# Optimization experiments

Measured on AMD Instinct MI355X. Metric: run time of the kernel, lower is better.

The kernel has to match this reference:

```python
import jax, jax.numpy as jnp
import numpy as np

N_NODES = 100000
N_EDGES = 1600000
DIM_IN, DIM_H, DIM_OUT = 128, 128, 64


def setup_inputs() -> dict:
    key = jax.random.key(0)
    ks = jax.random.split(key, 8)
    s = 0.05
    return {
        "x": jax.random.normal(ks[0], (N_NODES, DIM_IN), jnp.float32),
        "edge_index": jax.random.randint(ks[1], (2, N_EDGES), 0, N_NODES, jnp.int64),
        "W_l1": jax.random.normal(ks[2], (DIM_IN, DIM_H), jnp.float32) * s,
        "W_r1": jax.random.normal(ks[3], (DIM_IN, DIM_H), jnp.float32) * s,
        "b1": jax.random.normal(ks[4], (DIM_H,), jnp.float32) * s,
        "W_l2": jax.random.normal(ks[5], (DIM_H, DIM_OUT), jnp.float32) * s,
        "W_r2": jax.random.normal(ks[6], (DIM_H, DIM_OUT), jnp.float32) * s,
        "b2": jax.random.normal(ks[7], (DIM_OUT,), jnp.float32) * s,
    }


def _sage_conv(h, src, dst, n_nodes, W_l, W_r, b):
    # mean-aggregate neighbor features: gather x[src], scatter-sum to dst, divide by in-degree
    msg = h[src]                                              # [E, d]
    agg = jax.ops.segment_sum(msg, dst, num_segments=n_nodes)  # [N, d]
    deg = jax.ops.segment_sum(jnp.ones((src.shape[0],), h.dtype), dst, num_segments=n_nodes)
    mean = agg / jnp.maximum(deg, 1.0)[:, None]
    # out = lin_l(mean) + lin_r(x) ; bias lives on lin_l (PyG SAGEConv default)
    return mean @ W_l + h @ W_r + b


def reference(x, edge_index, W_l1, W_r1, b1, W_l2, W_r2, b2):
    src, dst = edge_index[0], edge_index[1]
    n = x.shape[0]
    h = jax.nn.relu(_sage_conv(x, src, dst, n, W_l1, W_r1, b1))
    # dropout(p=0.5) is identity in eval mode
    return _sage_conv(h, src, dst, n, W_l2, W_r2, b2)
```

## Files before the change

kernel.cpp:

```cpp
#include <hip/hip_runtime.h>

#define NN 100000
#define NE 1600000

typedef __attribute__((ext_vector_type(8))) short bf16x8;
typedef __attribute__((ext_vector_type(4))) float f32x4;

__device__ __forceinline__ float bf2f(unsigned short b) {
    union { unsigned int u; float f; } v;
    v.u = ((unsigned int)b) << 16;
    return v.f;
}
__device__ __forceinline__ unsigned short f2bf(float f) {
    union { float f; unsigned int u; } v; v.f = f;
    unsigned int u = v.u;
    return (unsigned short)((u + 0x7FFFu + ((u >> 16) & 1u)) >> 16);
}

__global__ void detect_kernel(const int* __restrict__ e, int* __restrict__ flag) {
    int t = blockIdx.x * blockDim.x + threadIdx.x;
    if (t < 4096 && e[2 * t + 1] != 0) atomicOr(flag, 1);
}

__device__ __forceinline__ int esrc(const int* e, int mode, int i) {
    return mode ? e[i] : e[2 * i];
}
__device__ __forceinline__ int edst(const int* e, int mode, int i) {
    return mode ? e[NE + i] : e[2 * (NE + i)];
}

#define NRANGE 4
#define RSZ 25000
#define NCHUNK 64
#define EPC (NE / NCHUNK)
#define GS 100352
#define RECCAP 8192

__global__ __launch_bounds__(512) void histA_kernel(
    const int* __restrict__ e, const int* __restrict__ flag,
    int* __restrict__ G, int2* __restrict__ recs, int* __restrict__ cnt) {
    __shared__ int lh[RSZ];
    __shared__ int lcnt;
    const int bid = blockIdx.x;
    const int r = bid & (NRANGE - 1);
    const int c = bid >> 2;
    const int lo = r * RSZ;
    for (int idx = threadIdx.x; idx < RSZ; idx += 512) lh[idx] = 0;
    if (threadIdx.x == 0) lcnt = 0;
    __syncthreads();
    const int mode = *flag;
    const int base = c * EPC;
    int2* __restrict__ myrec = recs + (size_t)bid * RECCAP;
    for (int i = base + threadIdx.x; i < base + EPC; i += 512) {
        int dl = edst(e, mode, i) - lo;
        if ((unsigned)dl < (unsigned)RSZ) {
            int s = esrc(e, mode, i);
            int p = atomicAdd(&lh[dl], 1);
            int slot = atomicAdd(&lcnt, 1);
            if (slot < RECCAP) myrec[slot] = make_int2(dl | (p << 15), s);
        }
    }
    __syncthreads();
    for (int idx = threadIdx.x; idx < RSZ; idx += 512)
        G[(size_t)c * GS + lo + idx] = lh[idx];
    if (threadIdx.x == 0) cnt[bid] = lcnt;
}

#define PREF_B 391
#define CVT_G 6250

__global__ __launch_bounds__(256) void prefix_cvt_kernel(
    int* __restrict__ G, int* __restrict__ S,
    const float* __restrict__ xin, unsigned short* __restrict__ xb) {
    if (blockIdx.x < PREF_B) {
        int d = blockIdx.x * 256 + threadIdx.x;
        if (d >= NN) return;
        int run = 0;
#pragma unroll 8
        for (int c = 0; c < NCHUNK; c++) {
            size_t idx = (size_t)c * GS + d;
            int t = G[idx];
            G[idx] = run;
            run += t;
        }
        S[d] = run;
    } else {
        long long i = ((long long)(blockIdx.x - PREF_B) * 256 + threadIdx.x) * 8;
        float4 a = *(const float4*)(xin + i);
        float4 b = *(const float4*)(xin + i + 4);
        bf16x8 rv;
        rv[0] = (short)f2bf(a.x); rv[1] = (short)f2bf(a.y);
        rv[2] = (short)f2bf(a.z); rv[3] = (short)f2bf(a.w);
        rv[4] = (short)f2bf(b.x); rv[5] = (short)f2bf(b.y);
        rv[6] = (short)f2bf(b.z); rv[7] = (short)f2bf(b.w);
        *(bf16x8*)(xb + i) = rv;
    }
}

#define SCAN_G 392

__global__ __launch_bounds__(256) void blocksum_kernel(const int* __restrict__ S,
                                                       int* __restrict__ part) {
    int i = blockIdx.x * 256 + threadIdx.x;
    int v = (i < NN) ? S[i] : 0;
#pragma unroll
    for (int off = 32; off; off >>= 1) v += __shfl_down(v, off, 64);
    __shared__ int wsum[4];
    if ((threadIdx.x & 63) == 0) wsum[threadIdx.x >> 6] = v;
    __syncthreads();
    if (threadIdx.x == 0)
        part[blockIdx.x] = wsum[0] + wsum[1] + wsum[2] + wsum[3];
}

__global__ __launch_bounds__(512) void partscan_kernel(int* __restrict__ part) {
    __shared__ int lds[512];
    const int t = threadIdx.x;
    int v = (t < SCAN_G) ? part[t] : 0;
    lds[t] = v;
    __syncthreads();
    for (int off = 1; off < 512; off <<= 1) {
        int u = (t >= off) ? lds[t - off] : 0;
        __syncthreads();
        lds[t] += u;
        __syncthreads();
    }
    if (t < SCAN_G) part[t] = lds[t] - v;
}

__global__ __launch_bounds__(256) void scanfin_kernel(int* __restrict__ S,
                                                      const int* __restrict__ part) {
    __shared__ int lds[256];
    const int t = threadIdx.x;
    const int i = blockIdx.x * 256 + t;
    int v = (i < NN) ? S[i] : 0;
    lds[t] = v;
    __syncthreads();
    for (int off = 1; off < 256; off <<= 1) {
        int u = (t >= off) ? lds[t - off] : 0;
        __syncthreads();
        lds[t] += u;
        __syncthreads();
    }
    if (i < NN) S[i] = lds[t] - v + part[blockIdx.x];
}

__global__ __launch_bounds__(512) void fillC_kernel(
    const int* __restrict__ S, const int* __restrict__ G,
    const int2* __restrict__ recs, const int* __restrict__ cnt,
    int* __restrict__ csr) {
    __shared__ int sOff[RSZ];
    const int bid = blockIdx.x;
    const int r = bid & (NRANGE - 1);
    const int c = bid >> 2;
    const int lo = r * RSZ;
    for (int idx = threadIdx.x; idx < RSZ; idx += 512)
        sOff[idx] = S[lo + idx] + G[(size_t)c * GS + lo + idx];
    __syncthreads();
    const int n = cnt[bid];
    const int2* __restrict__ myrec = recs + (size_t)bid * RECCAP;
    for (int k = threadIdx.x; k < n; k += 512) {
        int2 rec = myrec[k];
        int dl = rec.x & 0x7FFF;
        int p = rec.x >> 15;
        csr[sOff[dl] + p] = rec.y;
    }
}

template <int D>
__global__ __launch_bounds__(256) void gather_mean_bf16(
    const unsigned short* __restrict__ feat, const int* __restrict__ csr,
    const int* __restrict__ S, unsigned short* __restrict__ out) {
    constexpr int TPN = D / 8;
    constexpr int NPB = 256 / TPN;
    const int tid = threadIdx.x;
    const int node = blockIdx.x * NPB + tid / TPN;
    const int c = tid % TPN;
    if (node >= NN) return;
    const int begin = S[node];
    const int end = (node == NN - 1) ? NE : S[node + 1];
    float acc0[8] = {0.f, 0.f, 0.f, 0.f, 0.f, 0.f, 0.f, 0.f};
    float acc1[8] = {0.f, 0.f, 0.f, 0.f, 0.f, 0.f, 0.f, 0.f};
    int j = begin;
    for (; j + 4 <= end; j += 4) {
        int s0 = csr[j], s1 = csr[j + 1], s2 = csr[j + 2], s3 = csr[j + 3];
        bf16x8 v0 = *(const bf16x8*)(feat + (size_t)s0 * D + 8 * c);
        bf16x8 v1 = *(const bf16x8*)(feat + (size_t)s1 * D + 8 * c);
        bf16x8 v2 = *(const bf16x8*)(feat + (size_t)s2 * D + 8 * c);
        bf16x8 v3 = *(const bf16x8*)(feat + (size_t)s3 * D + 8 * c);
#pragma unroll
        for (int q = 0; q < 8; q++) {
            acc0[q] += bf2f((unsigned short)v0[q]) + bf2f((unsigned short)v2[q]);
            acc1[q] += bf2f((unsigned short)v1[q]) + bf2f((unsigned short)v3[q]);
        }
    }
    for (; j < end; j++) {
        int s = csr[j];
        bf16x8 v = *(const bf16x8*)(feat + (size_t)s * D + 8 * c);
#pragma unroll
        for (int q = 0; q < 8; q++) acc0[q] += bf2f((unsigned short)v[q]);
    }
    const float inv = 1.0f / fmaxf((float)(end - begin), 1.0f);
    bf16x8 r;
#pragma unroll
    for (int q = 0; q < 8; q++) r[q] = (short)f2bf((acc0[q] + acc1[q]) * inv);
    *(bf16x8*)(out + (size_t)node * D + 8 * c) = r;
}

template <int NO, bool DUAL, bool EADD, bool RELU, bool BIAS, bool OUTF32>
__global__ __launch_bounds__(256, 2) void mfma_gemm(
    const unsigned short* __restrict__ A,
    const unsigned short* __restrict__ X,
    const float* __restrict__ Wa,
    const float* __restrict__ Wb,
    const float* __restrict__ bias,
    const unsigned short* __restrict__ E,
    void* __restrict__ Yv, int N) {
    constexpr int NT = NO / 16;
    constexpr int PITCH = 136;
    __shared__ unsigned short sWb[NO * PITCH];
    __shared__ unsigned short sWa[DUAL ? NO * PITCH : 8];

    const int tid = threadIdx.x;
    for (int idx = tid; idx < 128 * NO; idx += 256) {
        int k = idx / NO, n = idx % NO;
        sWb[n * PITCH + k] = f2bf(Wb[idx]);
        if constexpr (DUAL) sWa[n * PITCH + k] = f2bf(Wa[idx]);
    }
    __syncthreads();

    const int lane = tid & 63;
    const int wv = tid >> 6;
    const int r16 = lane & 15;
    const int kg = lane >> 4;
    const long long rowbase = (long long)blockIdx.x * 128 + wv * 32;

    bf16x8 xf[2][4], af[2][4];
    const bf16x8 zz = {0, 0, 0, 0, 0, 0, 0, 0};
#pragma unroll
    for (int rt = 0; rt < 2; rt++) {
        long long row = rowbase + rt * 16 + r16;
        bool ok = row < N;
#pragma unroll
        for (int ks = 0; ks < 4; ks++) {
            xf[rt][ks] = ok ? *(const bf16x8*)(X + row * 128 + ks * 32 + kg * 8) : zz;
            if constexpr (DUAL)
                af[rt][ks] = ok ? *(const bf16x8*)(A + row * 128 + ks * 32 + kg * 8) : zz;
        }
    }

    f32x4 acc[2][NT];
#pragma unroll
    for (int t = 0; t < NT; t++) {
        float bv = 0.f;
        if constexpr (BIAS) bv = bias[t * 16 + r16];
#pragma unroll
        for (int rt = 0; rt < 2; rt++) acc[rt][t] = (f32x4){bv, bv, bv, bv};
    }

#pragma unroll
    for (int t = 0; t < NT; t++) {
        const unsigned short* wp = &sWb[(t * 16 + r16) * PITCH + kg * 8];
        bf16x8 bb[4];
#pragma unroll
        for (int ks = 0; ks < 4; ks++) bb[ks] = *(const bf16x8*)(wp + ks * 32);
        bf16x8 ba[4];
        if constexpr (DUAL) {
            const unsigned short* wq = &sWa[(t * 16 + r16) * PITCH + kg * 8];
#pragma unroll
            for (int ks = 0; ks < 4; ks++) ba[ks] = *(const bf16x8*)(wq + ks * 32);
        }
#pragma unroll
        for (int rt = 0; rt < 2; rt++) {
#pragma unroll
            for (int ks = 0; ks < 4; ks++) {
                acc[rt][t] = __builtin_amdgcn_mfma_f32_16x16x32_bf16(
                    xf[rt][ks], bb[ks], acc[rt][t], 0, 0, 0);
                if constexpr (DUAL)
                    acc[rt][t] = __builtin_amdgcn_mfma_f32_16x16x32_bf16(
                        af[rt][ks], ba[ks], acc[rt][t], 0, 0, 0);
            }
        }
    }

#pragma unroll
    for (int rt = 0; rt < 2; rt++) {
#pragma unroll
        for (int r = 0; r < 4; r++) {
            long long row = rowbase + rt * 16 + kg * 4 + r;
            if (row < N) {
#pragma unroll
                for (int t = 0; t < NT; t++) {
                    int col = t * 16 + r16;
                    float v = acc[rt][t][r];
                    if constexpr (EADD) v += bf2f(E[row * NO + col]);
                    if constexpr (RELU) v = fmaxf(v, 0.f);
                    if constexpr (OUTF32) ((float*)Yv)[row * NO + col] = v;
                    else ((unsigned short*)Yv)[row * NO + col] = f2bf(v);
                }
            }
        }
    }
}

extern "C" void kernel_launch(void* const* d_in, const int* in_sizes, int n_in,
                              void* d_out, int out_size, void* d_ws, size_t ws_size,
                              hipStream_t stream) {
    const float* x    = (const float*)d_in[0];
    const int*   e32  = (const int*)d_in[1];
    const float* W_l1 = (const float*)d_in[2];
    const float* W_r1 = (const float*)d_in[3];
    const float* b1   = (const float*)d_in[4];
    const float* W_l2 = (const float*)d_in[5];
    const float* W_r2 = (const float*)d_in[6];
    const float* b2   = (const float*)d_in[7];
    float* out = (float*)d_out;

    int* wsI = (int*)d_ws;
    int* flag = wsI;
    int* cnt  = wsI + 256;
    int* S    = wsI + 1024;
    int* part = wsI + 1024 + 100352;
    int* csr  = wsI + 101888;
    int2* recs = (int2*)(wsI + 1701888);
    unsigned short* xb = (unsigned short*)(wsI + 5896192);
    int* G = wsI + 12296192;
    unsigned short* mean1b = (unsigned short*)(wsI + 12296192);
    unsigned short* hb     = (unsigned short*)(wsI + 18696192);
    unsigned short* t2b    = xb;
    unsigned short* mean2b = xb + (size_t)NN * 64;

    hipMemsetAsync(d_ws, 0, 4096, stream);

    detect_kernel<<<16, 256, 0, stream>>>(e32, flag);
    histA_kernel<<<NRANGE * NCHUNK, 512, 0, stream>>>(e32, flag, G, recs, cnt);
    prefix_cvt_kernel<<<PREF_B + CVT_G, 256, 0, stream>>>(G, S, x, xb);
    blocksum_kernel<<<SCAN_G, 256, 0, stream>>>(S, part);
    partscan_kernel<<<1, 512, 0, stream>>>(part);
    scanfin_kernel<<<SCAN_G, 256, 0, stream>>>(S, part);
    fillC_kernel<<<NRANGE * NCHUNK, 512, 0, stream>>>(S, G, recs, cnt, csr);

    gather_mean_bf16<128><<<6250, 256, 0, stream>>>(xb, csr, S, mean1b);

    mfma_gemm<128, true, false, true, true, false>
        <<<782, 256, 0, stream>>>(mean1b, xb, W_l1, W_r1, b1, nullptr, hb, NN);

    mfma_gemm<64, false, false, false, false, false>
        <<<782, 256, 0, stream>>>(nullptr, hb, nullptr, W_l2, nullptr, nullptr, t2b, NN);

    gather_mean_bf16<64><<<3125, 256, 0, stream>>>(t2b, csr, S, mean2b);

    mfma_gemm<64, false, true, false, true, true>
        <<<782, 256, 0, stream>>>(nullptr, hb, nullptr, W_r2, b2, mean2b, out, NN);
}
```

Measured before the change: 235.1 us.

## Replace record buffer with re-read edge scatter and widen gather unroll

The histogram pass now only counts destination degrees, and a new scatter pass re-reads the edge list and places sources with LDS atomic offsets. This replaces the intermediate int2 record buffer and its extra write and read. Block size doubles to 1024 threads, and the mean-gather loop unrolls to 8 neighbors to keep more loads in flight. The catch is that the edge list is read twice, and neighbor order within each CSR row now depends on atomic order, so float summation order is no longer fixed.

```diff
diff --git a/kernel.cpp b/kernel.cpp
--- a/kernel.cpp
+++ b/kernel.cpp
@@ -34,36 +34,47 @@
 #define NCHUNK 64
 #define EPC (NE / NCHUNK)
 #define GS 100352
-#define RECCAP 8192
-
-__global__ __launch_bounds__(512) void histA_kernel(
-    const int* __restrict__ e, const int* __restrict__ flag,
-    int* __restrict__ G, int2* __restrict__ recs, int* __restrict__ cnt) {
+
+__global__ __launch_bounds__(1024) void histA_kernel(
+    const int* __restrict__ e, const int* __restrict__ flag, int* __restrict__ G) {
     __shared__ int lh[RSZ];
-    __shared__ int lcnt;
     const int bid = blockIdx.x;
     const int r = bid & (NRANGE - 1);
     const int c = bid >> 2;
     const int lo = r * RSZ;
-    for (int idx = threadIdx.x; idx < RSZ; idx += 512) lh[idx] = 0;
-    if (threadIdx.x == 0) lcnt = 0;
+    for (int idx = threadIdx.x; idx < RSZ; idx += 1024) lh[idx] = 0;
     __syncthreads();
     const int mode = *flag;
     const int base = c * EPC;
-    int2* __restrict__ myrec = recs + (size_t)bid * RECCAP;
-    for (int i = base + threadIdx.x; i < base + EPC; i += 512) {
+    for (int i = base + threadIdx.x; i < base + EPC; i += 1024) {
+        int dl = edst(e, mode, i) - lo;
+        if ((unsigned)dl < (unsigned)RSZ) atomicAdd(&lh[dl], 1);
+    }
+    __syncthreads();
+    for (int idx = threadIdx.x; idx < RSZ; idx += 1024)
+        G[(size_t)c * GS + lo + idx] = lh[idx];
+}
+
+__global__ __launch_bounds__(1024) void scatterC_kernel(
+    const int* __restrict__ e, const int* __restrict__ flag,
+    const int* __restrict__ S, const int* __restrict__ G, int* __restrict__ csr) {
+    __shared__ int sOff[RSZ];
+    const int bid = blockIdx.x;
+    const int r = bid & (NRANGE - 1);
+    const int c = bid >> 2;
+    const int lo = r * RSZ;
+    for (int idx = threadIdx.x; idx < RSZ; idx += 1024)
+        sOff[idx] = S[lo + idx] + G[(size_t)c * GS + lo + idx];
+    __syncthreads();
+    const int mode = *flag;
+    const int base = c * EPC;
+    for (int i = base + threadIdx.x; i < base + EPC; i += 1024) {
         int dl = edst(e, mode, i) - lo;
         if ((unsigned)dl < (unsigned)RSZ) {
             int s = esrc(e, mode, i);
-            int p = atomicAdd(&lh[dl], 1);
-            int slot = atomicAdd(&lcnt, 1);
-            if (slot < RECCAP) myrec[slot] = make_int2(dl | (p << 15), s);
-        }
-    }
-    __syncthreads();
-    for (int idx = threadIdx.x; idx < RSZ; idx += 512)
-        G[(size_t)c * GS + lo + idx] = lh[idx];
-    if (threadIdx.x == 0) cnt[bid] = lcnt;
+            csr[atomicAdd(&sOff[dl], 1)] = s;
+        }
+    }
 }
 
 #define PREF_B 391
@@ -142,28 +153,6 @@
         __syncthreads();
     }
     if (i < NN) S[i] = lds[t] - v + part[blockIdx.x];
-}
-
-__global__ __launch_bounds__(512) void fillC_kernel(
-    const int* __restrict__ S, const int* __restrict__ G,
-    const int2* __restrict__ recs, const int* __restrict__ cnt,
-    int* __restrict__ csr) {
-    __shared__ int sOff[RSZ];
-    const int bid = blockIdx.x;
-    const int r = bid & (NRANGE - 1);
-    const int c = bid >> 2;
-    const int lo = r * RSZ;
-    for (int idx = threadIdx.x; idx < RSZ; idx += 512)
-        sOff[idx] = S[lo + idx] + G[(size_t)c * GS + lo + idx];
-    __syncthreads();
-    const int n = cnt[bid];
-    const int2* __restrict__ myrec = recs + (size_t)bid * RECCAP;
-    for (int k = threadIdx.x; k < n; k += 512) {
-        int2 rec = myrec[k];
-        int dl = rec.x & 0x7FFF;
-        int p = rec.x >> 15;
-        csr[sOff[dl] + p] = rec.y;
-    }
 }
 
 template <int D>
@@ -181,19 +170,36 @@
     float acc0[8] = {0.f, 0.f, 0.f, 0.f, 0.f, 0.f, 0.f, 0.f};
     float acc1[8] = {0.f, 0.f, 0.f, 0.f, 0.f, 0.f, 0.f, 0.f};
     int j = begin;
-    for (; j + 4 <= end; j += 4) {
+    for (; j + 8 <= end; j += 8) {
         int s0 = csr[j], s1 = csr[j + 1], s2 = csr[j + 2], s3 = csr[j + 3];
+        int s4 = csr[j + 4], s5 = csr[j + 5], s6 = csr[j + 6], s7 = csr[j + 7];
         bf16x8 v0 = *(const bf16x8*)(feat + (size_t)s0 * D + 8 * c);
         bf16x8 v1 = *(const bf16x8*)(feat + (size_t)s1 * D + 8 * c);
         bf16x8 v2 = *(const bf16x8*)(feat + (size_t)s2 * D + 8 * c);
         bf16x8 v3 = *(const bf16x8*)(feat + (size_t)s3 * D + 8 * c);
+        bf16x8 v4 = *(const bf16x8*)(feat + (size_t)s4 * D + 8 * c);
+        bf16x8 v5 = *(const bf16x8*)(feat + (size_t)s5 * D + 8 * c);
+        bf16x8 v6 = *(const bf16x8*)(feat + (size_t)s6 * D + 8 * c);
+        bf16x8 v7 = *(const bf16x8*)(feat + (size_t)s7 * D + 8 * c);
 #pragma unroll
         for (int q = 0; q < 8; q++) {
-            acc0[q] += bf2f((unsigned short)v0[q]) + bf2f((unsigned short)v2[q]);
-            acc1[q] += bf2f((unsigned short)v1[q]) + bf2f((unsigned short)v3[q]);
-        }
-    }
-    for (; j < end; j++) {
+            acc0[q] += (bf2f((unsigned short)v0[q]) + bf2f((unsigned short)v2[q])) +
+                       (bf2f((unsigned short)v4[q]) + bf2f((unsigned short)v6[q]));
+            acc1[q] += (bf2f((unsigned short)v1[q]) + bf2f((unsigned short)v3[q])) +
+                       (bf2f((unsigned short)v5[q]) + bf2f((unsigned short)v7[q]));
+        }
+    }
+    for (; j + 2 <= end; j += 2) {
+        int s0 = csr[j], s1 = csr[j + 1];
+        bf16x8 v0 = *(const bf16x8*)(feat + (size_t)s0 * D + 8 * c);
+        bf16x8 v1 = *(const bf16x8*)(feat + (size_t)s1 * D + 8 * c);
+#pragma unroll
+        for (int q = 0; q < 8; q++) {
+            acc0[q] += bf2f((unsigned short)v0[q]);
+            acc1[q] += bf2f((unsigned short)v1[q]);
+        }
+    }
+    if (j < end) {
         int s = csr[j];
         bf16x8 v = *(const bf16x8*)(feat + (size_t)s * D + 8 * c);
 #pragma unroll
@@ -317,27 +323,25 @@
 
     int* wsI = (int*)d_ws;
     int* flag = wsI;
-    int* cnt  = wsI + 256;
     int* S    = wsI + 1024;
     int* part = wsI + 1024 + 100352;
     int* csr  = wsI + 101888;
-    int2* recs = (int2*)(wsI + 1701888);
-    unsigned short* xb = (unsigned short*)(wsI + 5896192);
-    int* G = wsI + 12296192;
-    unsigned short* mean1b = (unsigned short*)(wsI + 12296192);
-    unsigned short* hb     = (unsigned short*)(wsI + 18696192);
+    unsigned short* xb = (unsigned short*)(wsI + 1701888);
+    int* G = wsI + 8101888;
+    unsigned short* mean1b = (unsigned short*)(wsI + 8101888);
+    unsigned short* hb     = (unsigned short*)(wsI + 14524416);
     unsigned short* t2b    = xb;
     unsigned short* mean2b = xb + (size_t)NN * 64;
 
     hipMemsetAsync(d_ws, 0, 4096, stream);
 
     detect_kernel<<<16, 256, 0, stream>>>(e32, flag);
-    histA_kernel<<<NRANGE * NCHUNK, 512, 0, stream>>>(e32, flag, G, recs, cnt);
+    histA_kernel<<<NRANGE * NCHUNK, 1024, 0, stream>>>(e32, flag, G);
     prefix_cvt_kernel<<<PREF_B + CVT_G, 256, 0, stream>>>(G, S, x, xb);
     blocksum_kernel<<<SCAN_G, 256, 0, stream>>>(S, part);
     partscan_kernel<<<1, 512, 0, stream>>>(part);
     scanfin_kernel<<<SCAN_G, 256, 0, stream>>>(S, part);
-    fillC_kernel<<<NRANGE * NCHUNK, 512, 0, stream>>>(S, G, recs, cnt, csr);
+    scatterC_kernel<<<NRANGE * NCHUNK, 1024, 0, stream>>>(e32, flag, S, G, csr);
 
     gather_mean_bf16<128><<<6250, 256, 0, stream>>>(xb, csr, S, mean1b);
 
```

New measurement: 221.6 us. 1.06x faster.
